# Optimization experiments

Hardware: AMD Instinct MI355X
Metric: run time of the kernel (lower is better)

## Reference

```python
import jax, jax.numpy as jnp
import numpy as np

# Single-device reference: with head-parallel world size 1, both _SeqAllToAll
# collectives are identities, so the forward is exactly the kv-packed causal
# attention computed by loongtrain_attn_kvpacked_func (flash-attn semantics).

def setup_inputs() -> dict:
    key = jax.random.key(0)
    k1, k2 = jax.random.split(key)
    B, S, H, D = 1, 2048, 32, 128
    q = jax.random.normal(k1, (B, S, H, D), dtype=jnp.float32)
    kv = jax.random.normal(k2, (B, S, 2, H, D), dtype=jnp.float32)
    return {"q": q, "kv": kv}


def reference(q, kv) -> jnp.ndarray:
    # q: [B, S, H, D]; kv: [B, S, 2, H, D] (flash-attn kvpacked layout)
    B, S, H, D = q.shape
    k = kv[:, :, 0]  # [B, S, H, D]
    v = kv[:, :, 1]  # [B, S, H, D]
    scale = 1.0 / jnp.sqrt(jnp.asarray(D, dtype=q.dtype))
    # scores: [B, H, Sq, Sk]
    scores = jnp.einsum("bshd,bthd->bhst", q, k) * scale
    # causal mask (LoongTrain attention is causal)
    causal = jnp.tril(jnp.ones((S, S), dtype=bool))
    scores = jnp.where(causal[None, None, :, :], scores, jnp.asarray(-jnp.inf, dtype=scores.dtype))
    probs = jax.nn.softmax(scores, axis=-1)
    # context: [B, S, H, D]
    context = jnp.einsum("bhst,bthd->bshd", probs, v)
    return context
```

## Files before the change

### kernel.cpp

```cpp
#include <hip/hip_runtime.h>
#include <hip/hip_bf16.h>

typedef __bf16 bf16_t;
typedef __bf16 bf16x4 __attribute__((ext_vector_type(4)));
typedef __bf16 bf16x8 __attribute__((ext_vector_type(8)));
typedef float  f32x4  __attribute__((ext_vector_type(4)));

constexpr int S  = 2048;
constexpr int H  = 32;
constexpr int D  = 128;
constexpr int BR = 64;
constexpr int SC = 32;
constexpr int NT = S / BR;
constexpr int KSTR  = 136;
constexpr int VSTR2 = 20;

__device__ __forceinline__ bf16x8 cvt8(f32x4 lo, f32x4 hi) {
    bf16x8 r;
#pragma unroll
    for (int j = 0; j < 4; ++j) { r[j] = (bf16_t)lo[j]; r[4 + j] = (bf16_t)hi[j]; }
    return r;
}
__device__ __forceinline__ uint32_t pk2(float a, float b) {
    union { uint32_t u; bf16_t h[2]; } r;
    r.h[0] = (bf16_t)a; r.h[1] = (bf16_t)b;
    return r.u;
}

__global__ __launch_bounds__(256, 4)
void fa_fwd(const float* __restrict__ q, const float* __restrict__ kvp,
            float* __restrict__ out) {
    __shared__ __align__(16) bf16_t   Klds[2][SC * KSTR];
    __shared__ __align__(16) uint32_t Vt2[2][D * VSTR2];

    const int bx = blockIdx.x;
    const int h  = bx & 31;
    const int i  = bx >> 5;
    const int jg = i & 7, gi = i >> 3;
    const int qtile = (gi == 0) ? (31 - jg) : (gi == 1) ? jg
                     : (gi == 2) ? (23 - jg) : (8 + jg);
    const int q0    = qtile * BR;

    const int t    = threadIdx.x;
    const int w    = t >> 6;
    const int lane = t & 63;
    const int quad = lane >> 4;
    const int m    = lane & 15;

    const float sc = 0.08838834764831845f * 1.44269504088896340f;

    const int k2 = t >> 4, kc = t & 15;
    const int r0 = 2 * k2;
    const int lr0 = ((r0 >> 3) << 2) + (r0 & 3) + ((r0 & 4) ? 16 : 0);
    const size_t rowstep = (size_t)2 * H * D;
    const size_t tstep   = (size_t)SC * rowstep;
    const float* pk = kvp + (((size_t)r0 * 2 + 0) * H + h) * D + kc * 8;
    const float* pv = kvp + (((size_t)r0 * 2 + 1) * H + h) * D + kc * 8;
    const int vpos = k2 ^ ((kc & 3) << 2);
    const bool hb  = (kc & 4) != 0;

    const int qp0   = q0 + w * 16 + m;
    const int nkv   = (qtile + 1) * (BR / SC);
    const int qmaxw = q0 + w * 16 + 15;

    bf16x8 aq[4];
#pragma unroll
    for (int c = 0; c < 4; ++c) {
        const float* p = q + ((size_t)qp0 * H + h) * D + c * 32 + quad * 8;
        f32x4 lo = *(const f32x4*)p * sc;
        f32x4 hi = *(const f32x4*)(p + 4) * sc;
        aq[c] = cvt8(lo, hi);
    }

    f32x4 o[8];
#pragma unroll
    for (int idx = 0; idx < 8; ++idx) o[idx] = (f32x4)0.f;
    float lrow = 0.f;

    f32x4 kr[2][2], vr[2][2];
    auto ldregs = [&]() {
        kr[0][0] = *(const f32x4*)pk;             kr[0][1] = *(const f32x4*)(pk + 4);
        kr[1][0] = *(const f32x4*)(pk + rowstep); kr[1][1] = *(const f32x4*)(pk + rowstep + 4);
        vr[0][0] = *(const f32x4*)pv;             vr[0][1] = *(const f32x4*)(pv + 4);
        vr[1][0] = *(const f32x4*)(pv + rowstep); vr[1][1] = *(const f32x4*)(pv + rowstep + 4);
    };
    auto stage = [&](int b) {
        *(bf16x8*)&Klds[b][lr0       * KSTR + kc * 8] = cvt8(kr[0][0], kr[0][1]);
        *(bf16x8*)&Klds[b][(lr0 + 1) * KSTR + kc * 8] = cvt8(kr[1][0], kr[1][1]);
        f32x4 aA = hb ? vr[0][1] : vr[0][0];
        f32x4 bA = hb ? vr[1][1] : vr[1][0];
        f32x4 aB = hb ? vr[0][0] : vr[0][1];
        f32x4 bB = hb ? vr[1][0] : vr[1][1];
        const int dA = kc * 8 + (hb ? 4 : 0);
        const int dB = kc * 8 + (hb ? 0 : 4);
#pragma unroll
        for (int jq = 0; jq < 4; ++jq) {
            Vt2[b][(dA + jq) * VSTR2 + vpos] = pk2(aA[jq], bA[jq]);
            Vt2[b][(dB + jq) * VSTR2 + vpos] = pk2(aB[jq], bB[jq]);
        }
    };

    ldregs();
    stage(0);
    if (nkv > 1) { pk += tstep; pv += tstep; ldregs(); }
    __syncthreads();

    for (int kb = 0; kb < nkv; ++kb) {
        const int kv0 = kb * SC;
        const int cur = kb & 1;
        const bool active = (kv0 <= qmaxw);

        bf16x8 bp;
        if (active) {
            f32x4 sA[2];
            sA[0] = (f32x4)0.f; sA[1] = (f32x4)0.f;
            __builtin_amdgcn_s_setprio(1);
#pragma unroll
            for (int c = 0; c < 4; ++c) {
                bf16x8 ak0 = *(const bf16x8*)&Klds[cur][m * KSTR + c * 32 + quad * 8];
                bf16x8 ak1 = *(const bf16x8*)&Klds[cur][(16 + m) * KSTR + c * 32 + quad * 8];
                sA[0] = __builtin_amdgcn_mfma_f32_16x16x32_bf16(ak0, aq[c], sA[0], 0, 0, 0);
                sA[1] = __builtin_amdgcn_mfma_f32_16x16x32_bf16(ak1, aq[c], sA[1], 0, 0, 0);
            }
            __builtin_amdgcn_s_setprio(0);

            const int limb = q0 + w * 16 - kv0;
            float p[8], rs = 0.f;
            if (limb >= 31) {
#pragma unroll
                for (int r = 0; r < 4; ++r) {
                    p[r]     = __builtin_amdgcn_exp2f(fminf(sA[0][r], 80.f));
                    p[4 + r] = __builtin_amdgcn_exp2f(fminf(sA[1][r], 80.f));
                    rs += p[r] + p[4 + r];
                }
            } else {
                const int lim = limb + m;
#pragma unroll
                for (int r = 0; r < 4; ++r) {
                    float e0 = __builtin_amdgcn_exp2f(fminf(sA[0][r], 80.f));
                    float e1 = __builtin_amdgcn_exp2f(fminf(sA[1][r], 80.f));
                    p[r]     = (quad * 8 + r     <= lim) ? e0 : 0.f;
                    p[4 + r] = (quad * 8 + 4 + r <= lim) ? e1 : 0.f;
                    rs += p[r] + p[4 + r];
                }
            }
            lrow += rs;
#pragma unroll
            for (int r = 0; r < 4; ++r) { bp[r] = (bf16_t)p[r]; bp[4 + r] = (bf16_t)p[4 + r]; }
        }

        if (kb + 1 < nkv) {
            stage(cur ^ 1);
            if (kb + 2 < nkv) { pk += tstep; pv += tstep; ldregs(); }
        }

        if (active) {
            __builtin_amdgcn_s_setprio(1);
#pragma unroll
            for (int tt = 0; tt < 8; ++tt) {
                const int dd  = tt * 16 + m;
                const int grp = quad ^ ((dd >> 3) & 3);
                bf16x8 av = *(const bf16x8*)&Vt2[cur][dd * VSTR2 + grp * 4];
                o[tt] = __builtin_amdgcn_mfma_f32_16x16x32_bf16(av, bp, o[tt], 0, 0, 0);
            }
            __builtin_amdgcn_s_setprio(0);
        }
        __syncthreads();
    }

    lrow += __shfl_xor(lrow, 16);
    lrow += __shfl_xor(lrow, 32);

    {
        const float inv = 1.0f / lrow;
        float* op = out + ((size_t)qp0 * H + h) * D;
#pragma unroll
        for (int tt = 0; tt < 8; ++tt) {
            f32x4 val = o[tt] * inv;
            *(f32x4*)(op + tt * 16 + quad * 4) = val;
        }
    }
}

extern "C" void kernel_launch(void* const* d_in, const int* in_sizes, int n_in,
                              void* d_out, int out_size, void* d_ws, size_t ws_size,
                              hipStream_t stream) {
    const float* q  = (const float*)d_in[0];
    const float* kv = (const float*)d_in[1];
    float* out = (float*)d_out;
    dim3 grid(NT * H);
    dim3 block(256);
    fa_fwd<<<grid, block, 0, stream>>>(q, kv, out);
}
```

Before: 190.8 us.

## Double query tile to 128 rows with 512-thread blocks sharing each KV chunk

Raises the query tile from 64 to 128 rows and the block from 256 to 512 threads (8 waves), so each staged K/V chunk in LDS serves twice as many query rows, halving global KV traffic and conversion work per query. The staging loop is remapped so each thread loads half as much K and V, and the V transpose now uses one 4-wide column strip per thread. The tile-to-block schedule is simplified to fit 16 tiles. In exchange there are half as many blocks (512), so work per block is coarser and causal load balancing is worse, and waves_per_eu is fixed at 4.

```diff
diff --git a/kernel.cpp b/kernel.cpp
--- a/kernel.cpp
+++ b/kernel.cpp
@@ -2,14 +2,13 @@
 #include <hip/hip_bf16.h>
 
 typedef __bf16 bf16_t;
-typedef __bf16 bf16x4 __attribute__((ext_vector_type(4)));
 typedef __bf16 bf16x8 __attribute__((ext_vector_type(8)));
 typedef float  f32x4  __attribute__((ext_vector_type(4)));
 
 constexpr int S  = 2048;
 constexpr int H  = 32;
 constexpr int D  = 128;
-constexpr int BR = 64;
+constexpr int BR = 128;
 constexpr int SC = 32;
 constexpr int NT = S / BR;
 constexpr int KSTR  = 136;
@@ -27,7 +26,8 @@
     return r.u;
 }
 
-__global__ __launch_bounds__(256, 4)
+__global__ __launch_bounds__(512)
+__attribute__((amdgpu_waves_per_eu(4, 4)))
 void fa_fwd(const float* __restrict__ q, const float* __restrict__ kvp,
             float* __restrict__ out) {
     __shared__ __align__(16) bf16_t   Klds[2][SC * KSTR];
@@ -36,9 +36,7 @@
     const int bx = blockIdx.x;
     const int h  = bx & 31;
     const int i  = bx >> 5;
-    const int jg = i & 7, gi = i >> 3;
-    const int qtile = (gi == 0) ? (31 - jg) : (gi == 1) ? jg
-                     : (gi == 2) ? (23 - jg) : (8 + jg);
+    const int qtile = (i < 8) ? (15 - i) : (i - 8);
     const int q0    = qtile * BR;
 
     const int t    = threadIdx.x;
@@ -49,15 +47,17 @@
 
     const float sc = 0.08838834764831845f * 1.44269504088896340f;
 
-    const int k2 = t >> 4, kc = t & 15;
-    const int r0 = 2 * k2;
-    const int lr0 = ((r0 >> 3) << 2) + (r0 & 3) + ((r0 & 4) ? 16 : 0);
+    const int rk  = t >> 4;
+    const int kc  = t & 15;
+    const int lrk = ((rk >> 3) << 2) + (rk & 3) + ((rk & 4) ? 16 : 0);
+    const int vp  = t >> 5;
+    const int dh  = t & 31;
+    const int d0v = dh * 4;
+    const int vpos = vp ^ (((dh >> 1) & 3) << 2);
     const size_t rowstep = (size_t)2 * H * D;
     const size_t tstep   = (size_t)SC * rowstep;
-    const float* pk = kvp + (((size_t)r0 * 2 + 0) * H + h) * D + kc * 8;
-    const float* pv = kvp + (((size_t)r0 * 2 + 1) * H + h) * D + kc * 8;
-    const int vpos = k2 ^ ((kc & 3) << 2);
-    const bool hb  = (kc & 4) != 0;
+    const float* pk  = kvp + (((size_t)rk * 2 + 0) * H + h) * D + kc * 8;
+    const float* pv0 = kvp + (((size_t)(2 * vp) * 2 + 1) * H + h) * D + d0v;
 
     const int qp0   = q0 + w * 16 + m;
     const int nkv   = (qtile + 1) * (BR / SC);
@@ -77,32 +77,23 @@
     for (int idx = 0; idx < 8; ++idx) o[idx] = (f32x4)0.f;
     float lrow = 0.f;
 
-    f32x4 kr[2][2], vr[2][2];
+    f32x4 kr[2], vr0, vr1;
     auto ldregs = [&]() {
-        kr[0][0] = *(const f32x4*)pk;             kr[0][1] = *(const f32x4*)(pk + 4);
-        kr[1][0] = *(const f32x4*)(pk + rowstep); kr[1][1] = *(const f32x4*)(pk + rowstep + 4);
-        vr[0][0] = *(const f32x4*)pv;             vr[0][1] = *(const f32x4*)(pv + 4);
-        vr[1][0] = *(const f32x4*)(pv + rowstep); vr[1][1] = *(const f32x4*)(pv + rowstep + 4);
+        kr[0] = *(const f32x4*)pk;
+        kr[1] = *(const f32x4*)(pk + 4);
+        vr0   = *(const f32x4*)pv0;
+        vr1   = *(const f32x4*)(pv0 + rowstep);
     };
     auto stage = [&](int b) {
-        *(bf16x8*)&Klds[b][lr0       * KSTR + kc * 8] = cvt8(kr[0][0], kr[0][1]);
-        *(bf16x8*)&Klds[b][(lr0 + 1) * KSTR + kc * 8] = cvt8(kr[1][0], kr[1][1]);
-        f32x4 aA = hb ? vr[0][1] : vr[0][0];
-        f32x4 bA = hb ? vr[1][1] : vr[1][0];
-        f32x4 aB = hb ? vr[0][0] : vr[0][1];
-        f32x4 bB = hb ? vr[1][0] : vr[1][1];
-        const int dA = kc * 8 + (hb ? 4 : 0);
-        const int dB = kc * 8 + (hb ? 0 : 4);
+        *(bf16x8*)&Klds[b][lrk * KSTR + kc * 8] = cvt8(kr[0], kr[1]);
 #pragma unroll
-        for (int jq = 0; jq < 4; ++jq) {
-            Vt2[b][(dA + jq) * VSTR2 + vpos] = pk2(aA[jq], bA[jq]);
-            Vt2[b][(dB + jq) * VSTR2 + vpos] = pk2(aB[jq], bB[jq]);
-        }
+        for (int jq = 0; jq < 4; ++jq)
+            Vt2[b][(d0v + jq) * VSTR2 + vpos] = pk2(vr0[jq], vr1[jq]);
     };
 
     ldregs();
     stage(0);
-    if (nkv > 1) { pk += tstep; pv += tstep; ldregs(); }
+    if (nkv > 1) { pk += tstep; pv0 += tstep; ldregs(); }
     __syncthreads();
 
     for (int kb = 0; kb < nkv; ++kb) {
@@ -151,7 +142,7 @@
 
         if (kb + 1 < nkv) {
             stage(cur ^ 1);
-            if (kb + 2 < nkv) { pk += tstep; pv += tstep; ldregs(); }
+            if (kb + 2 < nkv) { pk += tstep; pv0 += tstep; ldregs(); }
         }
 
         if (active) {
@@ -189,6 +180,6 @@
     const float* kv = (const float*)d_in[1];
     float* out = (float*)d_out;
     dim3 grid(NT * H);
-    dim3 block(256);
+    dim3 block(512);
     fa_fwd<<<grid, block, 0, stream>>>(q, kv, out);
 }
```

After: 170.5 us. 1.12x faster.
